# Kernel optimization log

Hardware: AMD Instinct MI355X
Metric: run time of the kernel (lower is better)

The kernel has to match this reference:

```python
import jax, jax.numpy as jnp
import numpy as np

B, S, H, L = 4, 2048, 1024, 4
EPS = 1e-5
NEG = -1e9


def setup_inputs() -> dict:
    key = jax.random.key(0)
    ks = jax.random.split(key, 10)
    scale = 1.0 / np.sqrt(H)
    inp = {
        "x": jax.random.normal(ks[0], (B, S, H), dtype=jnp.float32),
        "mask": jnp.ones((B, 1, S), dtype=jnp.int32),
        # stacked per-layer params; torch Linear weight is [out, in]
        "Wq": jax.random.normal(ks[1], (L, H, H), dtype=jnp.float32) * scale,
        "bq": jnp.zeros((L, H), dtype=jnp.float32),
        "Wk": jax.random.normal(ks[2], (L, H, H), dtype=jnp.float32) * scale,
        "bk": jnp.zeros((L, H), dtype=jnp.float32),
        "Wv": jax.random.normal(ks[3], (L, H, H), dtype=jnp.float32) * scale,
        "bv": jnp.zeros((L, H), dtype=jnp.float32),
        "ln_w": jnp.ones((L, H), dtype=jnp.float32),
        "ln_b": jnp.zeros((L, H), dtype=jnp.float32),
    }
    return inp


def _layer(x, mask0, Wq, bq, Wk, bk, Wv, bv, ln_w, ln_b):
    # torch Linear: y = x @ W^T + b
    q = jnp.einsum("bsh,oh->bso", x, Wq) + bq
    k = jnp.einsum("bsh,oh->bso", x, Wk) + bk
    v = jnp.einsum("bsh,oh->bso", x, Wv) + bv
    inv_sqrt_h = jnp.asarray(1.0 / np.sqrt(H), x.dtype)
    scores = jnp.einsum("bsh,bth->bst", q, k) * inv_sqrt_h  # [B,S,S]
    scores = jnp.where(mask0, jnp.asarray(NEG, x.dtype), scores)
    probs = jax.nn.softmax(scores, axis=-1)
    attn = jnp.einsum("bst,bth->bsh", probs, v)
    # residual + LayerNorm (dropout is identity at eval)
    y = x + attn
    mu = jnp.mean(y, axis=-1, keepdims=True)
    var = jnp.mean(jnp.square(y - mu), axis=-1, keepdims=True)
    return ln_w * (y - mu) * jax.lax.rsqrt(var + EPS) + ln_b


def reference(x, mask, Wq, bq, Wk, bk, Wv, bv, ln_w, ln_b):
    mask0 = (mask == 0)  # [B,1,S], broadcasts over query dim
    for l in range(Wq.shape[0]):
        x = _layer(x, mask0, Wq[l], bq[l], Wk[l], bk[l], Wv[l], bv[l], ln_w[l], ln_b[l])
    return x
```

## Files before the change

kernel.cpp:

```cpp
#include <hip/hip_runtime.h>
#include <stdint.h>

typedef __bf16 bf16_t;
typedef __bf16 bf16x8 __attribute__((ext_vector_type(8)));
typedef __bf16 bf16x4 __attribute__((ext_vector_type(4)));
typedef float f32x4 __attribute__((ext_vector_type(4)));
typedef float f32x16 __attribute__((ext_vector_type(16)));
typedef unsigned int u32;

#define DEVINL static __device__ __forceinline__

constexpr int BB = 4;
constexpr int SEQ = 2048;
constexpr int HID = 1024;
constexpr int NL = 4;
constexpr int MR = BB * SEQ;
constexpr float LN_EPS = 1e-5f;

DEVINL f32x4 mfma16(bf16x8 a, bf16x8 b, f32x4 c) {
  return __builtin_amdgcn_mfma_f32_16x16x32_bf16(a, b, c, 0, 0, 0);
}
DEVINL f32x16 mfma32(bf16x8 a, bf16x8 b, f32x16 c) {
  return __builtin_amdgcn_mfma_f32_32x32x16_bf16(a, b, c, 0, 0, 0);
}

DEVINL void gload_lds16(const bf16_t* g, bf16_t* l) {
  __builtin_amdgcn_global_load_lds(
      (const __attribute__((address_space(1))) u32*)g,
      (__attribute__((address_space(3))) u32*)l, 16, 0, 0);
}

__global__ __launch_bounds__(512, 2) void gemm_qkv(
    const bf16_t* __restrict__ xb, const bf16_t* __restrict__ w0,
    const bf16_t* __restrict__ w1, const bf16_t* __restrict__ w2,
    const float* __restrict__ bias0, const float* __restrict__ bias1,
    const float* __restrict__ bias2, bf16_t* __restrict__ o0,
    bf16_t* __restrict__ o1, bf16_t* __restrict__ vT) {
  constexpr int BM = 256, BN = 128, NT = 16;

  __shared__ bf16_t smem[2 * BM * 64 + 2 * BN * 64];
  bf16_t* lA = smem;
  bf16_t* lB = smem + 2 * BM * 64;

  const int nwg = gridDim.x;
  int Lb = blockIdx.x;
  Lb = (Lb & 7) * (nwg >> 3) + (Lb >> 3);
  const int z = Lb >> 8;
  const int rem = Lb & 255;
  const int tm = rem >> 3;
  const int tn = rem & 7;
  const int brow = tm * BM, bcol = tn * BN;

  const bf16_t* B = (z == 0) ? w0 : (z == 1) ? w1 : w2;
  const float* bias = (z == 0) ? bias0 : (z == 1) ? bias1 : bias2;

  const int t = threadIdx.x, wave = t >> 6, lane = t & 63;
  const int wm = wave >> 1, wn = wave & 1;
  const int r31 = lane & 31, kb2 = lane >> 5;
  const int srow = t >> 3;
  const int cbk = (t & 7) ^ (srow & 7);
  const bf16_t* pAs = xb + (size_t)(brow + srow) * HID + cbk * 8;
  const bf16_t* pBs = B + (size_t)(bcol + srow) * HID + cbk * 8;
  bf16_t* lAw = lA + wave * 512;
  bf16_t* lBw = lB + wave * 512;

#define SA(X_, h_)                                                  \
  gload_lds16(pAs + (size_t)((h_)*64) * HID + (X_)*64,              \
              lAw + ((X_)&1) * (BM * 64) + (h_)*4096)
#define SB(X_, h_)                                                  \
  gload_lds16(pBs + (size_t)((h_)*64) * HID + (X_)*64,              \
              lBw + ((X_)&1) * (BN * 64) + (h_)*4096)

  const char* lAc = (const char*)lA;
  const char* lBc = (const char*)lB;
  int sX[4];
#pragma unroll
  for (int ks = 0; ks < 4; ++ks) sX[ks] = (((ks * 2 + kb2) ^ (r31 & 7)) << 4);
  const int rowA0 = wm * 64 + r31;
  const int rowB0 = wn * 64 + r31;

  f32x16 acc00 = {}, acc01 = {}, acc10 = {}, acc11 = {};

  SA(0, 0); SA(0, 1); SA(0, 2); SA(0, 3);
  SB(0, 0); SB(0, 1);
  SB(1, 0); SB(1, 1);
  asm volatile("s_waitcnt vmcnt(2)" ::: "memory");
  __builtin_amdgcn_s_barrier();

  for (int kt = 0; kt < NT; ++kt) {
    const char* aB = lAc + (kt & 1) * (BM * 128);
    const char* bB = lBc + (kt & 1) * (BN * 128);
    bf16x8 bF[2][4], a0[4];
#pragma unroll
    for (int ni = 0; ni < 2; ++ni)
#pragma unroll
      for (int ks = 0; ks < 4; ++ks)
        bF[ni][ks] = *(const bf16x8*)(bB + (rowB0 + ni * 32) * 128 + sX[ks]);
#pragma unroll
    for (int ks = 0; ks < 4; ++ks)
      a0[ks] = *(const bf16x8*)(aB + rowA0 * 128 + sX[ks]);
    if (kt + 1 < NT) { SA(kt + 1, 0); SA(kt + 1, 1); SA(kt + 1, 2); SA(kt + 1, 3); }
    __builtin_amdgcn_s_barrier();
    __builtin_amdgcn_s_setprio(1);
#pragma unroll
    for (int ks = 0; ks < 4; ++ks) {
      acc00 = mfma32(a0[ks], bF[0][ks], acc00);
      acc01 = mfma32(a0[ks], bF[1][ks], acc01);
    }
    __builtin_amdgcn_s_setprio(0);
    __builtin_amdgcn_s_barrier();
    bf16x8 a1[4];
#pragma unroll
    for (int ks = 0; ks < 4; ++ks)
      a1[ks] = *(const bf16x8*)(aB + (rowA0 + 32) * 128 + sX[ks]);
    if (kt + 2 < NT) { SB(kt + 2, 0); SB(kt + 2, 1); }
    __builtin_amdgcn_s_barrier();
    __builtin_amdgcn_s_setprio(1);
#pragma unroll
    for (int ks = 0; ks < 4; ++ks) {
      acc10 = mfma32(a1[ks], bF[0][ks], acc10);
      acc11 = mfma32(a1[ks], bF[1][ks], acc11);
    }
    __builtin_amdgcn_s_setprio(0);
    if (kt < NT - 2)
      asm volatile("s_waitcnt vmcnt(2)" ::: "memory");
    else
      asm volatile("s_waitcnt vmcnt(0)" ::: "memory");
    __builtin_amdgcn_s_barrier();
  }

  if (z < 2) {
    const int crow = brow + wm * 64 + 4 * kb2;
    const int ccol = bcol + wn * 64 + r31;
    bf16_t* outb = (z == 0) ? o0 : o1;
#pragma unroll
    for (int mi = 0; mi < 2; ++mi) {
#pragma unroll
      for (int ni = 0; ni < 2; ++ni) {
        const f32x16 av = (mi == 0) ? (ni == 0 ? acc00 : acc01)
                                    : (ni == 0 ? acc10 : acc11);
        const int col = ccol + ni * 32;
        const float badd = bias[col];
#pragma unroll
        for (int r = 0; r < 16; ++r) {
          const int row = crow + mi * 32 + (r & 3) + 8 * (r >> 2);
          outb[(size_t)row * HID + col] = (bf16_t)(av[r] + badd);
        }
      }
    }
  } else {
    bf16_t* tp = smem + wave * (64 * 72);
#pragma unroll
    for (int mi = 0; mi < 2; ++mi) {
#pragma unroll
      for (int ni = 0; ni < 2; ++ni) {
        const f32x16 av = (mi == 0) ? (ni == 0 ? acc00 : acc01)
                                    : (ni == 0 ? acc10 : acc11);
        const int cl = r31 + ni * 32;
        const float badd = bias[bcol + wn * 64 + cl];
#pragma unroll
        for (int g = 0; g < 4; ++g) {
          const int rl = mi * 32 + 8 * g + 4 * kb2;
          bf16x4 ov;
#pragma unroll
          for (int i = 0; i < 4; ++i) ov[i] = (bf16_t)(av[4 * g + i] + badd);
          *(bf16x4*)(tp + cl * 72 + rl) = ov;
        }
      }
    }
    asm volatile("s_waitcnt lgkmcnt(0)" ::: "memory");
    const int batch = brow >> 11;
    bf16_t* vt = vT + (size_t)batch * HID * SEQ;
    const int c0 = bcol + wn * 64;
    const int s0 = (brow & 2047) + wm * 64;
    const int lr = lane >> 3, lc = (lane & 7) * 8;
#pragma unroll
    for (int p = 0; p < 8; ++p) {
      const int rt = p * 8 + lr;
      const bf16x8 vv = *(const bf16x8*)(tp + rt * 72 + lc);
      *(bf16x8*)(vt + (size_t)(c0 + rt) * SEQ + s0 + lc) = vv;
    }
  }
#undef SA
#undef SB
}

__global__ __launch_bounds__(512, 2) void gemm_pv(
    const bf16_t* __restrict__ scores, const bf16_t* __restrict__ vT,
    const float* __restrict__ rsum, bf16_t* __restrict__ attn) {
  constexpr int BM = 256, BN = 128, NT = 32;

  __shared__ bf16_t smem[2 * BM * 64 + 2 * BN * 64];
  bf16_t* lA = smem;
  bf16_t* lB = smem + 2 * BM * 64;

  const int nwg = gridDim.x;
  int Lb = blockIdx.x;
  Lb = (Lb & 7) * (nwg >> 3) + (Lb >> 3);
  const int z = Lb >> 6;
  const int rem = Lb & 63;
  const int tm = rem >> 3;
  const int tn = rem & 7;
  const int brow = tm * BM, bcol = tn * BN;

  const bf16_t* A = scores + (size_t)z * SEQ * SEQ;
  const bf16_t* B = vT + (size_t)z * HID * SEQ;
  bf16_t* outb = attn + (size_t)z * SEQ * HID;

  const int t = threadIdx.x, wave = t >> 6, lane = t & 63;
  const int wm = wave >> 1, wn = wave & 1;
  const int r31 = lane & 31, kb2 = lane >> 5;
  const int srow = t >> 3;
  const int cbk = (t & 7) ^ (srow & 7);
  const bf16_t* pAs = A + (size_t)(brow + srow) * SEQ + cbk * 8;
  const bf16_t* pBs = B + (size_t)(bcol + srow) * SEQ + cbk * 8;
  bf16_t* lAw = lA + wave * 512;
  bf16_t* lBw = lB + wave * 512;

#define SA(X_, h_)                                                  \
  gload_lds16(pAs + (size_t)((h_)*64) * SEQ + (X_)*64,              \
              lAw + ((X_)&1) * (BM * 64) + (h_)*4096)
#define SB(X_, h_)                                                  \
  gload_lds16(pBs + (size_t)((h_)*64) * SEQ + (X_)*64,              \
              lBw + ((X_)&1) * (BN * 64) + (h_)*4096)

  const char* lAc = (const char*)lA;
  const char* lBc = (const char*)lB;
  int sX[4];
#pragma unroll
  for (int ks = 0; ks < 4; ++ks) sX[ks] = (((ks * 2 + kb2) ^ (r31 & 7)) << 4);
  const int rowA0 = wm * 64 + r31;
  const int rowB0 = wn * 64 + r31;

  f32x16 acc00 = {}, acc01 = {}, acc10 = {}, acc11 = {};

  SA(0, 0); SA(0, 1); SA(0, 2); SA(0, 3);
  SB(0, 0); SB(0, 1);
  SB(1, 0); SB(1, 1);
  asm volatile("s_waitcnt vmcnt(2)" ::: "memory");
  __builtin_amdgcn_s_barrier();

  for (int kt = 0; kt < NT; ++kt) {
    const char* aB = lAc + (kt & 1) * (BM * 128);
    const char* bB = lBc + (kt & 1) * (BN * 128);
    bf16x8 bF[2][4], a0[4];
#pragma unroll
    for (int ni = 0; ni < 2; ++ni)
#pragma unroll
      for (int ks = 0; ks < 4; ++ks)
        bF[ni][ks] = *(const bf16x8*)(bB + (rowB0 + ni * 32) * 128 + sX[ks]);
#pragma unroll
    for (int ks = 0; ks < 4; ++ks)
      a0[ks] = *(const bf16x8*)(aB + rowA0 * 128 + sX[ks]);
    if (kt + 1 < NT) { SA(kt + 1, 0); SA(kt + 1, 1); SA(kt + 1, 2); SA(kt + 1, 3); }
    __builtin_amdgcn_s_barrier();
    __builtin_amdgcn_s_setprio(1);
#pragma unroll
    for (int ks = 0; ks < 4; ++ks) {
      acc00 = mfma32(a0[ks], bF[0][ks], acc00);
      acc01 = mfma32(a0[ks], bF[1][ks], acc01);
    }
    __builtin_amdgcn_s_setprio(0);
    __builtin_amdgcn_s_barrier();
    bf16x8 a1[4];
#pragma unroll
    for (int ks = 0; ks < 4; ++ks)
      a1[ks] = *(const bf16x8*)(aB + (rowA0 + 32) * 128 + sX[ks]);
    if (kt + 2 < NT) { SB(kt + 2, 0); SB(kt + 2, 1); }
    __builtin_amdgcn_s_barrier();
    __builtin_amdgcn_s_setprio(1);
#pragma unroll
    for (int ks = 0; ks < 4; ++ks) {
      acc10 = mfma32(a1[ks], bF[0][ks], acc10);
      acc11 = mfma32(a1[ks], bF[1][ks], acc11);
    }
    __builtin_amdgcn_s_setprio(0);
    if (kt < NT - 2)
      asm volatile("s_waitcnt vmcnt(2)" ::: "memory");
    else
      asm volatile("s_waitcnt vmcnt(0)" ::: "memory");
    __builtin_amdgcn_s_barrier();
  }

  const float* rv = rsum + (size_t)z * SEQ;
  const int crow = brow + wm * 64 + 4 * kb2;
  const int ccol = bcol + wn * 64 + r31;
#pragma unroll
  for (int mi = 0; mi < 2; ++mi) {
#pragma unroll
    for (int ni = 0; ni < 2; ++ni) {
      const f32x16 av = (mi == 0) ? (ni == 0 ? acc00 : acc01)
                                  : (ni == 0 ? acc10 : acc11);
      const int col = ccol + ni * 32;
#pragma unroll
      for (int r = 0; r < 16; ++r) {
        const int row = crow + mi * 32 + (r & 3) + 8 * (r >> 2);
        outb[(size_t)row * HID + col] = (bf16_t)(av[r] / rv[row]);
      }
    }
  }
#undef SA
#undef SB
}

__global__ __launch_bounds__(512, 2) void gemm_qk(
    const bf16_t* __restrict__ Ab, const bf16_t* __restrict__ B0,
    const int* __restrict__ maskp, float* __restrict__ rsum,
    bf16_t* __restrict__ o0) {
  constexpr int TM = 8, TN = 8, NT = 16;

  __shared__ bf16_t lA[2 * 16384];
  __shared__ bf16_t lB[2 * 16384];

  const int nwg = gridDim.x;
  int Lb = blockIdx.x;
  Lb = (Lb & 7) * (nwg >> 3) + (Lb >> 3);
  const int z = Lb / (TM * TN);
  const int rem = Lb - z * (TM * TN);
  const int tm = rem / TN;
  const int tn = rem - tm * TN;
  const int brow = tm * 256, bcol = tn * 256;

  const bf16_t* A = Ab + (size_t)z * SEQ * HID;
  const bf16_t* B = B0 + (size_t)z * SEQ * HID;
  bf16_t* outb = o0 + (size_t)z * SEQ * SEQ;

  const int t = threadIdx.x, wave = t >> 6, lane = t & 63;
  const int wm = wave >> 2, wn = wave & 3;
  const int fr = lane & 15, kb = lane >> 4;
  const int srow = t >> 3;
  const int cbk = (t & 7) ^ (srow & 7);
  const bf16_t* pAs = A + (size_t)(brow + srow) * HID + cbk * 8;
  const bf16_t* pBs = B + (size_t)(bcol + srow) * HID + cbk * 8;
  bf16_t* lAw = lA + wave * 512;
  bf16_t* lBw = lB + wave * 512;

#define SA(X_, h_)                                                  \
  gload_lds16(pAs + (size_t)((h_)*64) * HID + (X_)*64,              \
              lAw + ((X_)&1) * 16384 + (h_)*4096)
#define SB(X_, h_)                                                  \
  gload_lds16(pBs + (size_t)((h_)*64) * HID + (X_)*64,              \
              lBw + ((X_)&1) * 16384 + (h_)*4096)

  const char* lAc = (const char*)lA;
  const char* lBc = (const char*)lB;
  const int cX0 = ((kb ^ (fr & 7)) << 4);
  const int cX1 = cX0 ^ 64;
  const int bRowOff = (wn & 1) * 64;

  f32x4 acc[8][4] = {};

  SA(0, 0); SA(0, 1); SA(0, 2); SA(0, 3);
  SB(0, 0); SB(0, 1); SB(0, 2); SB(0, 3);
  SA(1, 0); SA(1, 2);
  SB(1, 0); SB(1, 1); SB(1, 2); SB(1, 3);
  asm volatile("s_waitcnt vmcnt(6)" ::: "memory");
  __builtin_amdgcn_s_barrier();

  for (int kt = 0; kt < NT; ++kt) {
    const char* aB = lAc + (kt & 1) * 32768 + wm * 16384;
    const char* bB = lBc + (kt & 1) * 32768 + (wn >> 1) * 16384;
    bf16x8 bf_[4][2];
#pragma unroll
    for (int p = 0; p < 4; ++p) {
      if (p == 0) {
#pragma unroll
        for (int n = 0; n < 4; ++n) {
          const int rb = (bRowOff + n * 16 + fr) * 128;
          bf_[n][0] = *(const bf16x8*)(bB + rb + cX0);
          bf_[n][1] = *(const bf16x8*)(bB + rb + cX1);
        }
      }
      const int ra0 = (p * 32 + fr) * 128;
      const int ra1 = (p * 32 + 16 + fr) * 128;
      bf16x8 a00 = *(const bf16x8*)(aB + ra0 + cX0);
      bf16x8 a01 = *(const bf16x8*)(aB + ra0 + cX1);
      bf16x8 a10 = *(const bf16x8*)(aB + ra1 + cX0);
      bf16x8 a11 = *(const bf16x8*)(aB + ra1 + cX1);
      if (p == 0 && kt + 1 < NT) { SA(kt + 1, 1); SA(kt + 1, 3); }
      if (p == 1 && kt + 2 < NT) { SB(kt + 2, 0); SB(kt + 2, 1); }
      if (p == 2 && kt + 2 < NT) { SA(kt + 2, 0); SA(kt + 2, 2); }
      if (p == 3 && kt + 2 < NT) { SB(kt + 2, 2); SB(kt + 2, 3); }
      __builtin_amdgcn_s_barrier();
      __builtin_amdgcn_s_setprio(1);
#pragma unroll
      for (int n = 0; n < 4; ++n) {
        acc[2 * p][n] = mfma16(a00, bf_[n][0], acc[2 * p][n]);
        acc[2 * p][n] = mfma16(a01, bf_[n][1], acc[2 * p][n]);
        acc[2 * p + 1][n] = mfma16(a10, bf_[n][0], acc[2 * p + 1][n]);
        acc[2 * p + 1][n] = mfma16(a11, bf_[n][1], acc[2 * p + 1][n]);
      }
      __builtin_amdgcn_s_setprio(0);
      if (p == 3) {
        if (kt < NT - 3)
          asm volatile("s_waitcnt vmcnt(6)" ::: "memory");
        else
          asm volatile("s_waitcnt vmcnt(0)" ::: "memory");
      }
      __builtin_amdgcn_s_barrier();
    }
  }

  const int qr = lane >> 4;
  const int crow = brow + wm * 128 + qr * 4;
  const int ccol = bcol + wn * 64 + fr;
  const int* mrow = maskp + (size_t)z * SEQ;
  float* rs = rsum + (size_t)z * SEQ;
  int mv[4];
#pragma unroll
  for (int n = 0; n < 4; ++n) mv[n] = mrow[ccol + n * 16];
#pragma unroll
  for (int m = 0; m < 8; ++m) {
    const int row = crow + m * 16;
#pragma unroll
    for (int j = 0; j < 4; ++j) {
      float rp = 0.f;
#pragma unroll
      for (int n = 0; n < 4; ++n) {
        const int col = ccol + n * 16;
        const float p = mv[n] ? __expf(acc[m][n][j] * 0.03125f) : 0.f;
        outb[(size_t)(row + j) * SEQ + col] = (bf16_t)p;
        rp += p;
      }
      rp += __shfl_xor(rp, 1, 64);
      rp += __shfl_xor(rp, 2, 64);
      rp += __shfl_xor(rp, 4, 64);
      rp += __shfl_xor(rp, 8, 64);
      if (fr == 0) atomicAdd(&rs[row + j], rp);
    }
  }
#undef SA
#undef SB
}

__global__ __launch_bounds__(256) void cast4(
    const float* __restrict__ s0, const float* __restrict__ s1,
    const float* __restrict__ s2, const float* __restrict__ s3,
    bf16_t* __restrict__ d0, bf16_t* __restrict__ d1,
    bf16_t* __restrict__ d2, bf16_t* __restrict__ d3, long nW4, long nX4) {
  const int y = blockIdx.y;
  const float* in = (y == 0) ? s0 : (y == 1) ? s1 : (y == 2) ? s2 : s3;
  bf16_t* out = (y == 0) ? d0 : (y == 1) ? d1 : (y == 2) ? d2 : d3;
  const long n4 = (y == 3) ? nX4 : nW4;
  const long stride = (long)gridDim.x * blockDim.x;
  for (long i = (long)blockIdx.x * blockDim.x + threadIdx.x; i < n4;
       i += stride) {
    f32x4 x = *(const f32x4*)(in + i * 4);
    bf16x4 o;
#pragma unroll
    for (int j = 0; j < 4; ++j) o[j] = (bf16_t)x[j];
    *(bf16x4*)(out + i * 4) = o;
  }
}

__global__ __launch_bounds__(256) void resid_ln(
    const bf16_t* __restrict__ part0, const float* __restrict__ xinf,
    const bf16_t* __restrict__ xinb, const float* __restrict__ lnw,
    const float* __restrict__ lnb, float* __restrict__ xout,
    bf16_t* __restrict__ xbout) {
  const int row = blockIdx.x;
  const int t = threadIdx.x;
  const int wave = t >> 6;
  const int lane = t & 63;
  const size_t base = (size_t)row * HID + t * 4;
  const bf16x4 a0 = *(const bf16x4*)(part0 + base);
  f32x4 xv;
  if (xinf != nullptr) {
    xv = *(const f32x4*)(xinf + base);
  } else {
    const bf16x4 xbv = *(const bf16x4*)(xinb + base);
#pragma unroll
    for (int j = 0; j < 4; ++j) xv[j] = (float)xbv[j];
  }
  f32x4 y;
#pragma unroll
  for (int j = 0; j < 4; ++j) y[j] = (float)a0[j] + xv[j];
  float s1 = y[0] + y[1] + y[2] + y[3];
  float s2 = y[0] * y[0] + y[1] * y[1] + y[2] * y[2] + y[3] * y[3];
#pragma unroll
  for (int off = 32; off > 0; off >>= 1) {
    s1 += __shfl_xor(s1, off, 64);
    s2 += __shfl_xor(s2, off, 64);
  }
  __shared__ float red[8];
  if (lane == 0) {
    red[wave] = s1;
    red[4 + wave] = s2;
  }
  __syncthreads();
  s1 = red[0] + red[1] + red[2] + red[3];
  s2 = red[4] + red[5] + red[6] + red[7];
  const float mu = s1 * (1.f / HID);
  const float var = s2 * (1.f / HID) - mu * mu;
  const float rs = rsqrtf(var + LN_EPS);
  const f32x4 wv = *(const f32x4*)(lnw + t * 4);
  const f32x4 bv = *(const f32x4*)(lnb + t * 4);
  f32x4 o;
#pragma unroll
  for (int j = 0; j < 4; ++j) o[j] = wv[j] * ((y[j] - mu) * rs) + bv[j];
  if (xout != nullptr) *(f32x4*)(xout + base) = o;
  if (xbout != nullptr) {
    bf16x4 ob;
#pragma unroll
    for (int j = 0; j < 4; ++j) ob[j] = (bf16_t)o[j];
    *(bf16x4*)(xbout + base) = ob;
  }
}

extern "C" void kernel_launch(void* const* d_in, const int* in_sizes, int n_in,
                              void* d_out, int out_size, void* d_ws,
                              size_t ws_size, hipStream_t stream) {
  const float* x_in = (const float*)d_in[0];
  const int* mask = (const int*)d_in[1];
  const float* Wq = (const float*)d_in[2];
  const float* bq = (const float*)d_in[3];
  const float* Wk = (const float*)d_in[4];
  const float* bk = (const float*)d_in[5];
  const float* Wv = (const float*)d_in[6];
  const float* bv = (const float*)d_in[7];
  const float* lnw = (const float*)d_in[8];
  const float* lnb = (const float*)d_in[9];
  float* out = (float*)d_out;

  char* ws = (char*)d_ws;
  size_t off = 0;
  auto alloc = [&](size_t bytes) {
    char* p = ws + off;
    off += (bytes + 255) & ~(size_t)255;
    return (void*)p;
  };
  const size_t LHH = (size_t)NL * HID * HID;
  bf16_t* wqb = (bf16_t*)alloc(LHH * 2);
  bf16_t* wkb = (bf16_t*)alloc(LHH * 2);
  bf16_t* wvb = (bf16_t*)alloc(LHH * 2);
  bf16_t* xb = (bf16_t*)alloc((size_t)MR * HID * 2);
  bf16_t* q = (bf16_t*)alloc((size_t)MR * HID * 2);
  bf16_t* k = (bf16_t*)alloc((size_t)MR * HID * 2);
  bf16_t* vT = (bf16_t*)alloc((size_t)MR * HID * 2);
  bf16_t* scores = (bf16_t*)alloc((size_t)BB * SEQ * SEQ * 2);
  bf16_t* attn = (bf16_t*)alloc((size_t)MR * HID * 2);
  float* rsum = (float*)alloc((size_t)MR * 4);
  if (off > ws_size) return;

  cast4<<<dim3(1024, 4), 256, 0, stream>>>(Wq, Wk, Wv, x_in, wqb, wkb, wvb, xb,
                                           (long)(LHH / 4),
                                           (long)((size_t)MR * HID / 4));

  for (int l = 0; l < NL; ++l) {
    const size_t wo = (size_t)l * HID * HID;
    gemm_qkv<<<768, 512, 0, stream>>>(xb, wqb + wo, wkb + wo, wvb + wo,
                                      bq + (size_t)l * HID,
                                      bk + (size_t)l * HID,
                                      bv + (size_t)l * HID, q, k, vT);
    hipMemsetAsync(rsum, 0, (size_t)MR * 4, stream);
    gemm_qk<<<256, 512, 0, stream>>>(q, k, mask, rsum, scores);
    gemm_pv<<<256, 512, 0, stream>>>(scores, vT, rsum, attn);
    const float* xif = (l == 0) ? x_in : nullptr;
    float* xo = (l == NL - 1) ? out : nullptr;
    bf16_t* xbo = (l == NL - 1) ? nullptr : xb;
    resid_ln<<<MR, 256, 0, stream>>>(attn, xif, xb, lnw + (size_t)l * HID,
                                     lnb + (size_t)l * HID, xo, xbo);
  }
}
```

Before: 664.5 us.

## Swap GEMM kernels between QK and PV, split PV K-dimension into two halves

The QK^T score GEMM now uses the 256x128-tile 32x32 MFMA kernel with 512 workgroups instead of the 256x256 16x16 kernel. The PV GEMM moves to the 256x256 kernel with the sequence (K) dimension split in two, writing two partial attention outputs that resid_ln sums. This is meant to raise the workgroup count and give each GEMM a tile shape better matched to its dimensions. The cost is an extra MR x HID bf16 buffer to write and read, plus atomics spread over more, smaller tiles.

```diff
diff --git a/kernel.cpp b/kernel.cpp
--- a/kernel.cpp
+++ b/kernel.cpp
@@ -185,10 +185,11 @@
 #undef SB
 }
 
-__global__ __launch_bounds__(512, 2) void gemm_pv(
-    const bf16_t* __restrict__ scores, const bf16_t* __restrict__ vT,
-    const float* __restrict__ rsum, bf16_t* __restrict__ attn) {
-  constexpr int BM = 256, BN = 128, NT = 32;
+__global__ __launch_bounds__(512, 2) void gemm_qk32(
+    const bf16_t* __restrict__ q, const bf16_t* __restrict__ k,
+    const int* __restrict__ maskp, float* __restrict__ rsum,
+    bf16_t* __restrict__ scores) {
+  constexpr int BM = 256, BN = 128, NT = 16;
 
   __shared__ bf16_t smem[2 * BM * 64 + 2 * BN * 64];
   bf16_t* lA = smem;
@@ -197,31 +198,31 @@
   const int nwg = gridDim.x;
   int Lb = blockIdx.x;
   Lb = (Lb & 7) * (nwg >> 3) + (Lb >> 3);
-  const int z = Lb >> 6;
-  const int rem = Lb & 63;
-  const int tm = rem >> 3;
-  const int tn = rem & 7;
+  const int z = Lb >> 7;
+  const int rem = Lb & 127;
+  const int tm = rem >> 4;
+  const int tn = rem & 15;
   const int brow = tm * BM, bcol = tn * BN;
 
-  const bf16_t* A = scores + (size_t)z * SEQ * SEQ;
-  const bf16_t* B = vT + (size_t)z * HID * SEQ;
-  bf16_t* outb = attn + (size_t)z * SEQ * HID;
+  const bf16_t* A = q + (size_t)z * SEQ * HID;
+  const bf16_t* B = k + (size_t)z * SEQ * HID;
+  bf16_t* outb = scores + (size_t)z * SEQ * SEQ;
 
   const int t = threadIdx.x, wave = t >> 6, lane = t & 63;
   const int wm = wave >> 1, wn = wave & 1;
   const int r31 = lane & 31, kb2 = lane >> 5;
   const int srow = t >> 3;
   const int cbk = (t & 7) ^ (srow & 7);
-  const bf16_t* pAs = A + (size_t)(brow + srow) * SEQ + cbk * 8;
-  const bf16_t* pBs = B + (size_t)(bcol + srow) * SEQ + cbk * 8;
+  const bf16_t* pAs = A + (size_t)(brow + srow) * HID + cbk * 8;
+  const bf16_t* pBs = B + (size_t)(bcol + srow) * HID + cbk * 8;
   bf16_t* lAw = lA + wave * 512;
   bf16_t* lBw = lB + wave * 512;
 
 #define SA(X_, h_)                                                  \
-  gload_lds16(pAs + (size_t)((h_)*64) * SEQ + (X_)*64,              \
+  gload_lds16(pAs + (size_t)((h_)*64) * HID + (X_)*64,              \
               lAw + ((X_)&1) * (BM * 64) + (h_)*4096)
 #define SB(X_, h_)                                                  \
-  gload_lds16(pBs + (size_t)((h_)*64) * SEQ + (X_)*64,              \
+  gload_lds16(pBs + (size_t)((h_)*64) * HID + (X_)*64,              \
               lBw + ((X_)&1) * (BN * 64) + (h_)*4096)
 
   const char* lAc = (const char*)lA;
@@ -282,32 +283,41 @@
     __builtin_amdgcn_s_barrier();
   }
 
-  const float* rv = rsum + (size_t)z * SEQ;
   const int crow = brow + wm * 64 + 4 * kb2;
   const int ccol = bcol + wn * 64 + r31;
+  const int* mrow = maskp + (size_t)z * SEQ;
+  float* rs = rsum + (size_t)z * SEQ;
+  const int mv0 = mrow[ccol];
+  const int mv1 = mrow[ccol + 32];
 #pragma unroll
   for (int mi = 0; mi < 2; ++mi) {
-#pragma unroll
-    for (int ni = 0; ni < 2; ++ni) {
-      const f32x16 av = (mi == 0) ? (ni == 0 ? acc00 : acc01)
-                                  : (ni == 0 ? acc10 : acc11);
-      const int col = ccol + ni * 32;
-#pragma unroll
-      for (int r = 0; r < 16; ++r) {
-        const int row = crow + mi * 32 + (r & 3) + 8 * (r >> 2);
-        outb[(size_t)row * HID + col] = (bf16_t)(av[r] / rv[row]);
-      }
+    const f32x16 a0v = (mi == 0) ? acc00 : acc10;
+    const f32x16 a1v = (mi == 0) ? acc01 : acc11;
+#pragma unroll
+    for (int r = 0; r < 16; ++r) {
+      const int row = crow + mi * 32 + (r & 3) + 8 * (r >> 2);
+      const float p0 = mv0 ? __expf(a0v[r] * 0.03125f) : 0.f;
+      const float p1 = mv1 ? __expf(a1v[r] * 0.03125f) : 0.f;
+      outb[(size_t)row * SEQ + ccol] = (bf16_t)p0;
+      outb[(size_t)row * SEQ + ccol + 32] = (bf16_t)p1;
+      float rp = p0 + p1;
+      rp += __shfl_xor(rp, 1, 64);
+      rp += __shfl_xor(rp, 2, 64);
+      rp += __shfl_xor(rp, 4, 64);
+      rp += __shfl_xor(rp, 8, 64);
+      rp += __shfl_xor(rp, 16, 64);
+      if (r31 == 0) atomicAdd(&rs[row], rp);
     }
   }
 #undef SA
 #undef SB
 }
 
-__global__ __launch_bounds__(512, 2) void gemm_qk(
-    const bf16_t* __restrict__ Ab, const bf16_t* __restrict__ B0,
-    const int* __restrict__ maskp, float* __restrict__ rsum,
-    bf16_t* __restrict__ o0) {
-  constexpr int TM = 8, TN = 8, NT = 16;
+__global__ __launch_bounds__(512, 2) void gemm_pv2(
+    const bf16_t* __restrict__ scores, const bf16_t* __restrict__ vT,
+    const float* __restrict__ rsum, bf16_t* __restrict__ o0,
+    bf16_t* __restrict__ o1) {
+  constexpr int TM = 8, TN = 4, NT = 16;
 
   __shared__ bf16_t lA[2 * 16384];
   __shared__ bf16_t lB[2 * 16384];
@@ -321,25 +331,26 @@
   const int tn = rem - tm * TN;
   const int brow = tm * 256, bcol = tn * 256;
 
-  const bf16_t* A = Ab + (size_t)z * SEQ * HID;
-  const bf16_t* B = B0 + (size_t)z * SEQ * HID;
-  bf16_t* outb = o0 + (size_t)z * SEQ * SEQ;
+  const int zb = z >> 1, kh = z & 1;
+  const bf16_t* A = scores + (size_t)zb * SEQ * SEQ + kh * 1024;
+  const bf16_t* B = vT + (size_t)zb * HID * SEQ + kh * 1024;
+  bf16_t* outb = ((kh == 0) ? o0 : o1) + (size_t)zb * SEQ * HID;
 
   const int t = threadIdx.x, wave = t >> 6, lane = t & 63;
   const int wm = wave >> 2, wn = wave & 3;
   const int fr = lane & 15, kb = lane >> 4;
   const int srow = t >> 3;
   const int cbk = (t & 7) ^ (srow & 7);
-  const bf16_t* pAs = A + (size_t)(brow + srow) * HID + cbk * 8;
-  const bf16_t* pBs = B + (size_t)(bcol + srow) * HID + cbk * 8;
+  const bf16_t* pAs = A + (size_t)(brow + srow) * SEQ + cbk * 8;
+  const bf16_t* pBs = B + (size_t)(bcol + srow) * SEQ + cbk * 8;
   bf16_t* lAw = lA + wave * 512;
   bf16_t* lBw = lB + wave * 512;
 
 #define SA(X_, h_)                                                  \
-  gload_lds16(pAs + (size_t)((h_)*64) * HID + (X_)*64,              \
+  gload_lds16(pAs + (size_t)((h_)*64) * SEQ + (X_)*64,              \
               lAw + ((X_)&1) * 16384 + (h_)*4096)
 #define SB(X_, h_)                                                  \
-  gload_lds16(pBs + (size_t)((h_)*64) * HID + (X_)*64,              \
+  gload_lds16(pBs + (size_t)((h_)*64) * SEQ + (X_)*64,              \
               lBw + ((X_)&1) * 16384 + (h_)*4096)
 
   const char* lAc = (const char*)lA;
@@ -401,32 +412,21 @@
     }
   }
 
+  const float* rv = rsum + (size_t)zb * SEQ;
   const int qr = lane >> 4;
   const int crow = brow + wm * 128 + qr * 4;
   const int ccol = bcol + wn * 64 + fr;
-  const int* mrow = maskp + (size_t)z * SEQ;
-  float* rs = rsum + (size_t)z * SEQ;
-  int mv[4];
-#pragma unroll
-  for (int n = 0; n < 4; ++n) mv[n] = mrow[ccol + n * 16];
 #pragma unroll
   for (int m = 0; m < 8; ++m) {
     const int row = crow + m * 16;
 #pragma unroll
     for (int j = 0; j < 4; ++j) {
-      float rp = 0.f;
+      const float ri = 1.f / rv[row + j];
 #pragma unroll
       for (int n = 0; n < 4; ++n) {
         const int col = ccol + n * 16;
-        const float p = mv[n] ? __expf(acc[m][n][j] * 0.03125f) : 0.f;
-        outb[(size_t)(row + j) * SEQ + col] = (bf16_t)p;
-        rp += p;
+        outb[(size_t)(row + j) * HID + col] = (bf16_t)(acc[m][n][j] * ri);
       }
-      rp += __shfl_xor(rp, 1, 64);
-      rp += __shfl_xor(rp, 2, 64);
-      rp += __shfl_xor(rp, 4, 64);
-      rp += __shfl_xor(rp, 8, 64);
-      if (fr == 0) atomicAdd(&rs[row + j], rp);
     }
   }
 #undef SA
@@ -454,16 +454,17 @@
 }
 
 __global__ __launch_bounds__(256) void resid_ln(
-    const bf16_t* __restrict__ part0, const float* __restrict__ xinf,
-    const bf16_t* __restrict__ xinb, const float* __restrict__ lnw,
-    const float* __restrict__ lnb, float* __restrict__ xout,
-    bf16_t* __restrict__ xbout) {
+    const bf16_t* __restrict__ part0, const bf16_t* __restrict__ part1,
+    const float* __restrict__ xinf, const bf16_t* __restrict__ xinb,
+    const float* __restrict__ lnw, const float* __restrict__ lnb,
+    float* __restrict__ xout, bf16_t* __restrict__ xbout) {
   const int row = blockIdx.x;
   const int t = threadIdx.x;
   const int wave = t >> 6;
   const int lane = t & 63;
   const size_t base = (size_t)row * HID + t * 4;
   const bf16x4 a0 = *(const bf16x4*)(part0 + base);
+  const bf16x4 a1 = *(const bf16x4*)(part1 + base);
   f32x4 xv;
   if (xinf != nullptr) {
     xv = *(const f32x4*)(xinf + base);
@@ -474,7 +475,7 @@
   }
   f32x4 y;
 #pragma unroll
-  for (int j = 0; j < 4; ++j) y[j] = (float)a0[j] + xv[j];
+  for (int j = 0; j < 4; ++j) y[j] = (float)a0[j] + (float)a1[j] + xv[j];
   float s1 = y[0] + y[1] + y[2] + y[3];
   float s2 = y[0] * y[0] + y[1] * y[1] + y[2] * y[2] + y[3] * y[3];
 #pragma unroll
@@ -538,7 +539,8 @@
   bf16_t* k = (bf16_t*)alloc((size_t)MR * HID * 2);
   bf16_t* vT = (bf16_t*)alloc((size_t)MR * HID * 2);
   bf16_t* scores = (bf16_t*)alloc((size_t)BB * SEQ * SEQ * 2);
-  bf16_t* attn = (bf16_t*)alloc((size_t)MR * HID * 2);
+  bf16_t* attn0 = (bf16_t*)alloc((size_t)MR * HID * 2);
+  bf16_t* attn1 = (bf16_t*)alloc((size_t)MR * HID * 2);
   float* rsum = (float*)alloc((size_t)MR * 4);
   if (off > ws_size) return;
 
@@ -553,12 +555,13 @@
                                       bk + (size_t)l * HID,
                                       bv + (size_t)l * HID, q, k, vT);
     hipMemsetAsync(rsum, 0, (size_t)MR * 4, stream);
-    gemm_qk<<<256, 512, 0, stream>>>(q, k, mask, rsum, scores);
-    gemm_pv<<<256, 512, 0, stream>>>(scores, vT, rsum, attn);
+    gemm_qk32<<<512, 512, 0, stream>>>(q, k, mask, rsum, scores);
+    gemm_pv2<<<256, 512, 0, stream>>>(scores, vT, rsum, attn0, attn1);
     const float* xif = (l == 0) ? x_in : nullptr;
     float* xo = (l == NL - 1) ? out : nullptr;
     bf16_t* xbo = (l == NL - 1) ? nullptr : xb;
-    resid_ln<<<MR, 256, 0, stream>>>(attn, xif, xb, lnw + (size_t)l * HID,
+    resid_ln<<<MR, 256, 0, stream>>>(attn0, attn1, xif, xb,
+                                     lnw + (size_t)l * HID,
                                      lnb + (size_t)l * HID, xo, xbo);
   }
 }
```

Result: slower. 719.0 us (+8.2%).
